# Performance work log

Measured on AMD Instinct MI355X. Metric: run time of the kernel, lower is better.

Reference implementation:

```python
import jax, jax.numpy as jnp
import numpy as np

K = 10  # value-iteration steps


def _conv(x, w):
    # NCHW x OIHW -> NCHW, stride 1, SAME padding (pad=2 for 5x5, pad=0 for 1x1)
    return jax.lax.conv_general_dilated(
        x, w, window_strides=(1, 1), padding='SAME',
        dimension_numbers=('NCHW', 'OIHW', 'NCHW'))


def setup_inputs() -> dict:
    key = jax.random.key(0)
    ks = jax.random.split(key, 6)
    B, H, W = 64, 64, 64
    dim_h, n_hat, n_act = 150, 8, 4
    maze = jax.random.randint(ks[0], (B, H, W), 0, 3)
    # fixed embedding table from the torch module
    emb = jnp.array([[0.0, 0.0], [1.0, 0.0], [0.0, 10.0]], dtype=jnp.float32)
    encode_w = jax.random.normal(ks[1], (dim_h, 2, 5, 5), dtype=jnp.float32) * 0.05
    encode_b = jnp.zeros((dim_h,), dtype=jnp.float32)
    r_w = jax.random.normal(ks[2], (1, dim_h, 1, 1), dtype=jnp.float32) * 0.05
    q_w = jax.random.normal(ks[3], (n_hat, 1, 5, 5), dtype=jnp.float32) * 0.05
    # torch inits self.w to zeros; use small randn so the recurrence is non-trivial
    w = jax.random.normal(ks[4], (n_hat, 1, 5, 5), dtype=jnp.float32) * 0.05
    fc_w = jax.random.normal(ks[5], (n_act, n_hat), dtype=jnp.float32) * 0.1
    return dict(maze=maze, emb=emb, encode_w=encode_w, encode_b=encode_b,
                r_w=r_w, q_w=q_w, w=w, fc_w=fc_w)


def reference(maze, emb, encode_w, encode_b, r_w, q_w, w, fc_w):
    # embed: [B,H,W] -> [B,H,W,2] -> [B,2,H,W]
    m = emb[maze].transpose(0, 3, 1, 2)
    h = _conv(m, encode_w) + encode_b[None, :, None, None]  # [B,150,H,W]
    r = _conv(h, r_w)                                        # [B,1,H,W]
    q = _conv(r, q_w)                                        # [B,8,H,W]
    wk = jnp.concatenate([q_w, w], axis=1)                   # [8,2,5,5]

    def step(q, _):
        v = jnp.max(q, axis=1, keepdims=True)                # [B,1,H,W]
        q = _conv(jnp.concatenate([r, v], axis=1), wk)       # [B,8,H,W]
        return q, None

    q, _ = jax.lax.scan(step, q, None, length=K)
    q = q.transpose(0, 2, 3, 1)                              # [B,H,W,8]
    return q @ fc_w.T                                        # [B,H,W,4]
```

## Files before the change

kernel.cpp:

```cpp
#include <hip/hip_runtime.h>
#include <hip/hip_bf16.h>


#define NHAT 8
#define DIMH 150
#define OWN 16

typedef float v2f __attribute__((ext_vector_type(2)));

__global__ __launch_bounds__(256) void rq_kernel(
    const int* __restrict__ maze, const float* __restrict__ emb,
    const float* __restrict__ encode_w, const float* __restrict__ encode_b,
    const float* __restrict__ r_w, const float* __restrict__ q_w,
    float* __restrict__ q0g) {
  __shared__ float wpart[250];
  __shared__ float bpart[152];
  __shared__ float weff[2][25];
  __shared__ float bsh;
  __shared__ float Ts[4][25];
  __shared__ v2f qw2[25][4];
  __shared__ unsigned char mzt[24][68];
  __shared__ float rt[20][68];

  int tid = threadIdx.x;
  int b = blockIdx.y, A0 = blockIdx.x * OWN;

  for (int i = tid; i < 24 * 68; i += 256) {
    int mr = i / 68, mc = i % 68;
    int gy = A0 - 4 + mr, gx = mc - 2;
    unsigned char v = 3;
    if (gy >= 0 && gy < 64 && gx >= 0 && gx < 64)
      v = (unsigned char)maze[(b * 64 + gy) * 64 + gx];
    mzt[mr][mc] = v;
  }
  if (tid < 100) {
    int k = tid >> 2, j = tid & 3;
    qw2[k][j] = (v2f){q_w[(2 * j) * 25 + k], q_w[(2 * j + 1) * 25 + k]};
  }
  if (tid < 250) {
    int ik = tid % 50, chunk = tid / 50;
    int i = ik / 25, k = ik % 25;
    int c0 = chunk * 30;
    float s = 0.f;
    for (int c = c0; c < c0 + 30; ++c)
      s += r_w[c] * encode_w[c * 50 + i * 25 + k];
    wpart[tid] = s;
  }
  if (tid < 150) bpart[tid] = r_w[tid] * encode_b[tid];
  __syncthreads();
  if (tid < 50) {
    float s = 0.f;
    for (int ch = 0; ch < 5; ++ch) s += wpart[ch * 50 + tid];
    weff[tid / 25][tid % 25] = s;
  }
  if (tid == 50) {
    float s = 0.f;
    for (int c = 0; c < 150; ++c) s += bpart[c];
    bsh = s;
  }
  __syncthreads();
  if (tid < 100) {
    int val = tid / 25, k = tid % 25;
    float t = 0.f;
    if (val < 3) t = weff[0][k] * emb[val * 2] + weff[1][k] * emb[val * 2 + 1];
    Ts[val][k] = t;
  }
  __syncthreads();
  for (int i = tid; i < 20 * 68; i += 256) {
    int rr = i / 68, cc = i % 68;
    int gy = A0 - 2 + rr, gx = cc - 2;
    float v = 0.f;
    if (gy >= 0 && gy < 64 && gx >= 0 && gx < 64) {
      v = bsh;
#pragma unroll
      for (int ky = 0; ky < 5; ++ky)
#pragma unroll
        for (int kx = 0; kx < 5; ++kx)
          v += Ts[mzt[rr + ky][cc - 2 + kx]][ky * 5 + kx];
    }
    rt[rr][cc] = v;
  }
  __syncthreads();
  for (int i = tid; i < OWN * 64; i += 256) {
    int ly = i >> 6, gx = i & 63;
    int gy = A0 + ly;
    v2f acc[4];
#pragma unroll
    for (int j = 0; j < 4; ++j) acc[j] = (v2f){0.f, 0.f};
#pragma unroll
    for (int ky = 0; ky < 5; ++ky)
#pragma unroll
      for (int kx = 0; kx < 5; ++kx) {
        int k = ky * 5 + kx;
        float vv = rt[ly + ky][gx + kx];
        v2f vv2 = (v2f){vv, vv};
#pragma unroll
        for (int j = 0; j < 4; ++j) acc[j] += qw2[k][j] * vv2;
      }
    float* dst = q0g + ((size_t)(b * 4096 + gy * 64 + gx)) * NHAT;
    ((float4*)dst)[0] = make_float4(acc[0].x, acc[0].y, acc[1].x, acc[1].y);
    ((float4*)dst)[1] = make_float4(acc[2].x, acc[2].y, acc[3].x, acc[3].y);
  }
}

__global__ __launch_bounds__(512, 2) void vi_kernel(
    const float* __restrict__ q0g, const float* __restrict__ w,
    const float* __restrict__ fc_w, float* __restrict__ out) {
  __shared__ float vbuf[2][64][68];
  __shared__ v2f wl2[25][4];
  __shared__ float fcs[4][NHAT];

  int tid = threadIdx.x;
  int b = blockIdx.y, a0 = blockIdx.x * OWN;
  int wave = tid >> 6, gx = tid & 63;

  if (tid < 100) {
    int k = tid >> 2, j = tid & 3;
    wl2[k][j] = (v2f){w[(2 * j) * 25 + k], w[(2 * j + 1) * 25 + k]};
  } else if (tid >= 128 && tid < 160) {
    int t = tid - 128;
    fcs[t >> 3][t & 7] = fc_w[t];
  }
  for (int i = tid; i < 2 * 64 * 68; i += 512) ((float*)vbuf)[i] = 0.f;
  __syncthreads();

  v2f wr[4][25];
#pragma unroll
  for (int k = 0; k < 25; ++k) {
#pragma unroll
    for (int j = 0; j < 4; ++j) wr[j][k] = wl2[k][j];
  }

  const float* q0b = q0g + (size_t)b * 4096 * NHAT;
  int cur = 0;

  {
    int s = max(0, a0 - 20), e = min(64, a0 + OWN + 20);
    for (int r = s + wave; r < e; r += 8) {
      const float4* p = (const float4*)(q0b + ((size_t)r * 64 + gx) * NHAT);
      float4 f0 = p[0], f1 = p[1];
      float m = fmaxf(fmaxf(fmaxf(f0.x, f0.y), fmaxf(f0.z, f0.w)),
                      fmaxf(fmaxf(f1.x, f1.y), fmaxf(f1.z, f1.w)));
      vbuf[0][r - a0 + 22][gx + 2] = m;
    }
  }
  __syncthreads();

  for (int t = 1; t <= 10; ++t) {
    int hh = 2 * (10 - t);
    int s = max(0, a0 - hh), e = min(64, a0 + OWN + hh);
    for (int r = s + wave; r < e; r += 8) {
      int lr = r - a0 + 22;
      const float4* p = (const float4*)(q0b + ((size_t)r * 64 + gx) * NHAT);
      float4 f0 = p[0], f1 = p[1];
      v2f a0v = (v2f){0.f, 0.f}, a1v = (v2f){0.f, 0.f};
      v2f a2v = (v2f){0.f, 0.f}, a3v = (v2f){0.f, 0.f};
#pragma unroll
      for (int ky = 0; ky < 5; ++ky) {
        const float* row = &vbuf[cur][lr - 2 + ky][gx];
#pragma unroll
        for (int kx = 0; kx < 5; ++kx) {
          int k = ky * 5 + kx;
          float vv = row[kx];
          v2f vv2 = (v2f){vv, vv};
          a0v += wr[0][k] * vv2;
          a1v += wr[1][k] * vv2;
          a2v += wr[2][k] * vv2;
          a3v += wr[3][k] * vv2;
        }
      }
      a0v += (v2f){f0.x, f0.y};
      a1v += (v2f){f0.z, f0.w};
      a2v += (v2f){f1.x, f1.y};
      a3v += (v2f){f1.z, f1.w};
      if (t < 10) {
        float m = fmaxf(fmaxf(fmaxf(a0v.x, a0v.y), fmaxf(a1v.x, a1v.y)),
                        fmaxf(fmaxf(a2v.x, a2v.y), fmaxf(a3v.x, a3v.y)));
        vbuf[cur ^ 1][lr][gx + 2] = m;
      } else {
        float4 o;
        float* op = &o.x;
#pragma unroll
        for (int a = 0; a < 4; ++a) {
          op[a] = fcs[a][0] * a0v.x + fcs[a][1] * a0v.y + fcs[a][2] * a1v.x +
                  fcs[a][3] * a1v.y + fcs[a][4] * a2v.x + fcs[a][5] * a2v.y +
                  fcs[a][6] * a3v.x + fcs[a][7] * a3v.y;
        }
        *(float4*)&out[((size_t)((b * 64 + r) * 64 + gx)) * 4] = o;
      }
    }
    cur ^= 1;
    if (t < 10) __syncthreads();
  }
}

extern "C" void kernel_launch(void* const* d_in, const int* in_sizes, int n_in,
                              void* d_out, int out_size, void* d_ws, size_t ws_size,
                              hipStream_t stream) {
  const int* maze = (const int*)d_in[0];
  const float* emb = (const float*)d_in[1];
  const float* encode_w = (const float*)d_in[2];
  const float* encode_b = (const float*)d_in[3];
  const float* r_w = (const float*)d_in[4];
  const float* q_w = (const float*)d_in[5];
  const float* w = (const float*)d_in[6];
  const float* fc_w = (const float*)d_in[7];
  float* out = (float*)d_out;

  float* q0 = (float*)d_ws;

  dim3 grid(4, 64);
  rq_kernel<<<grid, 256, 0, stream>>>(maze, emb, encode_w, encode_b, r_w, q_w, q0);
  vi_kernel<<<grid, 512, 0, stream>>>(q0, w, fc_w, out);
}
```

Measured before the change: 124.4 us.

## Split weight folding into prep kernel and halve VI tile height for more blocks

The folded encoder/reward weights are now computed once by a new single-block prep kernel instead of redundantly in every rq block, and rq loads the precomputed table. The value-iteration kernel now owns 8 rows per block instead of 16, doubling the grid to 512 blocks. The halo stays 20 rows, so the shared buffer shrinks but the redundant halo recomputation per owned row roughly doubles. VI weights are loaded straight from global into registers. The extra launch adds a small serial step before rq.

```diff
diff --git a/kernel.cpp b/kernel.cpp
--- a/kernel.cpp
+++ b/kernel.cpp
@@ -4,27 +4,56 @@
 
 #define NHAT 8
 #define DIMH 150
-#define OWN 16
 
 typedef float v2f __attribute__((ext_vector_type(2)));
 
+__global__ __launch_bounds__(128) void prep_kernel(
+    const float* __restrict__ emb, const float* __restrict__ encode_w,
+    const float* __restrict__ encode_b, const float* __restrict__ r_w,
+    float* __restrict__ T, float* __restrict__ beff) {
+  __shared__ float weff[2][25];
+  int tid = threadIdx.x;
+  if (tid < 50) {
+    int i = tid / 25, k = tid % 25;
+    float s = 0.f;
+    for (int c = 0; c < DIMH; ++c)
+      s += r_w[c] * encode_w[c * 50 + i * 25 + k];
+    weff[i][k] = s;
+  }
+  if (tid == 64) {
+    float s = 0.f;
+    for (int c = 0; c < DIMH; ++c) s += r_w[c] * encode_b[c];
+    *beff = s;
+  }
+  __syncthreads();
+  if (tid < 100) {
+    int val = tid / 25, k = tid % 25;
+    float t = 0.f;
+    if (val < 3) t = weff[0][k] * emb[val * 2] + weff[1][k] * emb[val * 2 + 1];
+    T[val * 25 + k] = t;
+  }
+}
+
 __global__ __launch_bounds__(256) void rq_kernel(
-    const int* __restrict__ maze, const float* __restrict__ emb,
-    const float* __restrict__ encode_w, const float* __restrict__ encode_b,
-    const float* __restrict__ r_w, const float* __restrict__ q_w,
+    const int* __restrict__ maze, const float* __restrict__ Tg,
+    const float* __restrict__ beffg, const float* __restrict__ q_w,
     float* __restrict__ q0g) {
-  __shared__ float wpart[250];
-  __shared__ float bpart[152];
-  __shared__ float weff[2][25];
+  __shared__ float Ts[4][25];
   __shared__ float bsh;
-  __shared__ float Ts[4][25];
   __shared__ v2f qw2[25][4];
   __shared__ unsigned char mzt[24][68];
   __shared__ float rt[20][68];
 
   int tid = threadIdx.x;
-  int b = blockIdx.y, A0 = blockIdx.x * OWN;
-
+  int b = blockIdx.y, A0 = blockIdx.x * 16;
+
+  if (tid < 100) Ts[tid / 25][tid % 25] = Tg[tid];
+  if (tid == 100) bsh = *beffg;
+  if (tid >= 128 && tid < 228) {
+    int t2 = tid - 128;
+    int k = t2 >> 2, j = t2 & 3;
+    qw2[k][j] = (v2f){q_w[(2 * j) * 25 + k], q_w[(2 * j + 1) * 25 + k]};
+  }
   for (int i = tid; i < 24 * 68; i += 256) {
     int mr = i / 68, mc = i % 68;
     int gy = A0 - 4 + mr, gx = mc - 2;
@@ -33,38 +62,6 @@
       v = (unsigned char)maze[(b * 64 + gy) * 64 + gx];
     mzt[mr][mc] = v;
   }
-  if (tid < 100) {
-    int k = tid >> 2, j = tid & 3;
-    qw2[k][j] = (v2f){q_w[(2 * j) * 25 + k], q_w[(2 * j + 1) * 25 + k]};
-  }
-  if (tid < 250) {
-    int ik = tid % 50, chunk = tid / 50;
-    int i = ik / 25, k = ik % 25;
-    int c0 = chunk * 30;
-    float s = 0.f;
-    for (int c = c0; c < c0 + 30; ++c)
-      s += r_w[c] * encode_w[c * 50 + i * 25 + k];
-    wpart[tid] = s;
-  }
-  if (tid < 150) bpart[tid] = r_w[tid] * encode_b[tid];
-  __syncthreads();
-  if (tid < 50) {
-    float s = 0.f;
-    for (int ch = 0; ch < 5; ++ch) s += wpart[ch * 50 + tid];
-    weff[tid / 25][tid % 25] = s;
-  }
-  if (tid == 50) {
-    float s = 0.f;
-    for (int c = 0; c < 150; ++c) s += bpart[c];
-    bsh = s;
-  }
-  __syncthreads();
-  if (tid < 100) {
-    int val = tid / 25, k = tid % 25;
-    float t = 0.f;
-    if (val < 3) t = weff[0][k] * emb[val * 2] + weff[1][k] * emb[val * 2 + 1];
-    Ts[val][k] = t;
-  }
   __syncthreads();
   for (int i = tid; i < 20 * 68; i += 256) {
     int rr = i / 68, cc = i % 68;
@@ -81,7 +78,7 @@
     rt[rr][cc] = v;
   }
   __syncthreads();
-  for (int i = tid; i < OWN * 64; i += 256) {
+  for (int i = tid; i < 16 * 64; i += 256) {
     int ly = i >> 6, gx = i & 63;
     int gy = A0 + ly;
     v2f acc[4];
@@ -106,51 +103,47 @@
 __global__ __launch_bounds__(512, 2) void vi_kernel(
     const float* __restrict__ q0g, const float* __restrict__ w,
     const float* __restrict__ fc_w, float* __restrict__ out) {
-  __shared__ float vbuf[2][64][68];
-  __shared__ v2f wl2[25][4];
+  __shared__ float vbuf[2][48][68];
   __shared__ float fcs[4][NHAT];
 
   int tid = threadIdx.x;
-  int b = blockIdx.y, a0 = blockIdx.x * OWN;
+  int b = blockIdx.y, a0 = blockIdx.x * 8;
   int wave = tid >> 6, gx = tid & 63;
 
-  if (tid < 100) {
-    int k = tid >> 2, j = tid & 3;
-    wl2[k][j] = (v2f){w[(2 * j) * 25 + k], w[(2 * j + 1) * 25 + k]};
-  } else if (tid >= 128 && tid < 160) {
+  if (tid >= 128 && tid < 160) {
     int t = tid - 128;
     fcs[t >> 3][t & 7] = fc_w[t];
   }
-  for (int i = tid; i < 2 * 64 * 68; i += 512) ((float*)vbuf)[i] = 0.f;
-  __syncthreads();
+  for (int i = tid; i < 2 * 48 * 68; i += 512) ((float*)vbuf)[i] = 0.f;
 
   v2f wr[4][25];
 #pragma unroll
-  for (int k = 0; k < 25; ++k) {
-#pragma unroll
-    for (int j = 0; j < 4; ++j) wr[j][k] = wl2[k][j];
-  }
+  for (int j = 0; j < 4; ++j)
+#pragma unroll
+    for (int k = 0; k < 25; ++k)
+      wr[j][k] = (v2f){w[(2 * j) * 25 + k], w[(2 * j + 1) * 25 + k]};
+  __syncthreads();
 
   const float* q0b = q0g + (size_t)b * 4096 * NHAT;
   int cur = 0;
 
   {
-    int s = max(0, a0 - 20), e = min(64, a0 + OWN + 20);
+    int s = max(0, a0 - 20), e = min(64, a0 + 28);
     for (int r = s + wave; r < e; r += 8) {
       const float4* p = (const float4*)(q0b + ((size_t)r * 64 + gx) * NHAT);
       float4 f0 = p[0], f1 = p[1];
       float m = fmaxf(fmaxf(fmaxf(f0.x, f0.y), fmaxf(f0.z, f0.w)),
                       fmaxf(fmaxf(f1.x, f1.y), fmaxf(f1.z, f1.w)));
-      vbuf[0][r - a0 + 22][gx + 2] = m;
+      vbuf[0][r - a0 + 20][gx + 2] = m;
     }
   }
   __syncthreads();
 
   for (int t = 1; t <= 10; ++t) {
     int hh = 2 * (10 - t);
-    int s = max(0, a0 - hh), e = min(64, a0 + OWN + hh);
+    int s = max(0, a0 - hh), e = min(64, a0 + 8 + hh);
     for (int r = s + wave; r < e; r += 8) {
-      int lr = r - a0 + 22;
+      int lr = r - a0 + 20;
       const float4* p = (const float4*)(q0b + ((size_t)r * 64 + gx) * NHAT);
       float4 f0 = p[0], f1 = p[1];
       v2f a0v = (v2f){0.f, 0.f}, a1v = (v2f){0.f, 0.f};
@@ -207,9 +200,12 @@
   const float* fc_w = (const float*)d_in[7];
   float* out = (float*)d_out;
 
-  float* q0 = (float*)d_ws;
-
-  dim3 grid(4, 64);
-  rq_kernel<<<grid, 256, 0, stream>>>(maze, emb, encode_w, encode_b, r_w, q_w, q0);
-  vi_kernel<<<grid, 512, 0, stream>>>(q0, w, fc_w, out);
-}
+  float* wsf = (float*)d_ws;
+  float* T = wsf;
+  float* beff = wsf + 100;
+  float* q0 = wsf + 128;
+
+  prep_kernel<<<1, 128, 0, stream>>>(emb, encode_w, encode_b, r_w, T, beff);
+  rq_kernel<<<dim3(4, 64), 256, 0, stream>>>(maze, T, beff, q_w, q0);
+  vi_kernel<<<dim3(8, 64), 512, 0, stream>>>(q0, w, fc_w, out);
+}
```

After: 176.4 us. +41.8%, slower.
